# Kernel optimization log

Measured on AMD Instinct MI355X. Metric: run time of the kernel, lower is better.

The kernel has to match this reference:

```python
import jax, jax.numpy as jnp
import numpy as np

B, H, W, C = 8, 56, 56, 192
HEADS, K, PAD = 6, 3, 1
KK = K * K
HEAD_DIM = C // HEADS
SCALE = HEAD_DIM ** -0.5


def setup_inputs() -> dict:
    key = jax.random.key(0)
    ks = jax.random.split(key, 6)
    s = lambda fan_in: 1.0 / np.sqrt(fan_in)
    return {
        "x": jax.random.normal(ks[0], (B, H, W, C), jnp.float32),
        "Wv": jax.random.normal(ks[1], (C, C), jnp.float32) * s(C),
        "Wa": jax.random.normal(ks[2], (C, KK * KK * HEADS), jnp.float32) * s(C),
        "ba": jax.random.normal(ks[3], (KK * KK * HEADS,), jnp.float32) * s(C),
        "Wp": jax.random.normal(ks[4], (C, C), jnp.float32) * s(C),
        "bp": jax.random.normal(ks[5], (C,), jnp.float32) * s(C),
    }


def _unfold(v_nchw):
    # im2col, kernel 3, pad 1, stride 1 -> (B, C, 9, H, W); kernel pos row-major like nn.Unfold
    vp = jnp.pad(v_nchw, ((0, 0), (0, 0), (PAD, PAD), (PAD, PAD)))
    return jnp.stack([vp[:, :, i:i + H, j:j + W] for i in range(K) for j in range(K)], axis=2)


def _fold(cols):
    # col2im scatter-add: cols (B, C, 9, H, W) -> (B, C, H, W)
    out = jnp.zeros((cols.shape[0], cols.shape[1], H + 2 * PAD, W + 2 * PAD), cols.dtype)
    idx = 0
    for i in range(K):
        for j in range(K):
            out = out.at[:, :, i:i + H, j:j + W].add(cols[:, :, idx])
            idx += 1
    return out[:, :, PAD:PAD + H, PAD:PAD + W]


def reference(x, Wv, Wa, ba, Wp, bp):
    hw = H * W
    # values: linear then unfold into per-pixel kxk windows
    v = jnp.einsum("bhwc,cd->bhwd", x, Wv)              # (B,H,W,C)
    v = _unfold(v.transpose(0, 3, 1, 2))                 # (B,C,9,H,W)
    v = v.reshape(B, HEADS, HEAD_DIM, KK, hw)
    v = v.transpose(0, 1, 4, 3, 2)                       # (B,heads,HW,9,c)
    # dynamic attention weights (stride=1 -> pool is identity)
    a = jnp.einsum("bhwc,ck->bhwk", x, Wa) + ba          # (B,H,W,81*heads)
    a = a.reshape(B, hw, HEADS, KK, KK).transpose(0, 2, 1, 3, 4)
    a = jax.nn.softmax(a * SCALE, axis=-1)               # (B,heads,HW,9,9)
    o = jnp.einsum("bnpkl,bnplc->bnpkc", a, v)           # (B,heads,HW,9,c)
    o = o.transpose(0, 1, 4, 3, 2).reshape(B, C, KK, H, W)
    o = _fold(o)                                          # (B,C,H,W)
    o = o.transpose(0, 2, 3, 1)                           # NHWC
    return jnp.einsum("bhwc,cd->bhwd", o, Wp) + bp
```

## Files before the change

kernel.cpp:

```cpp
#include <hip/hip_runtime.h>
#include <hip/hip_bf16.h>

constexpr int NH = 56, NW = 56, NC = 192, AJ = 486;
constexpr int HWP = NH * NW;
constexpr int NPIX = 8 * HWP;
constexpr float SCALE = 0.17677669529663687f;
constexpr int TS = 12288;

typedef __bf16 bf16x8 __attribute__((ext_vector_type(8)));
typedef float f32x4 __attribute__((ext_vector_type(4)));

__device__ __forceinline__ void gload16(const void* g, void* l) {
  __builtin_amdgcn_global_load_lds(
      (const __attribute__((address_space(1))) void*)g,
      (__attribute__((address_space(3))) void*)l, 16, 0, 0);
}

__device__ __forceinline__ size_t toff(int row, int k) {
  return (size_t)(row >> 6) * TS + (k >> 5) * 2048 + (row & 63) * 32 + (k & 31);
}

__global__ __launch_bounds__(256) void k_prep3(const float* __restrict__ x,
                                               const float* __restrict__ Wv,
                                               const float* __restrict__ Wa,
                                               const float* __restrict__ Wp,
                                               __bf16* __restrict__ xb,
                                               __bf16* __restrict__ Wvt,
                                               __bf16* __restrict__ Wat,
                                               __bf16* __restrict__ Wpt) {
  const int bid = blockIdx.x;
  if (bid < 144) {
    const int i = bid * 256 + threadIdx.x;
    const int n = i / 192, k = i - n * 192;
    const size_t d = toff(n, k);
    Wvt[d] = (__bf16)Wv[k * 192 + n];
    Wpt[d] = (__bf16)Wp[k * 192 + n];
  } else if (bid < 528) {
    const int i = (bid - 144) * 256 + threadIdx.x;
    const int n = i / 192, k = i - n * 192;
    Wat[toff(n, k)] = (n < 486) ? (__bf16)Wa[k * 486 + n] : (__bf16)0.f;
  } else {
    const size_t i = (size_t)(bid - 528) * 256 + threadIdx.x;
    const int pix = (int)(i / 24), c8 = (int)(i % 24) * 8;
    const float* src = x + (size_t)pix * 192 + c8;
    const float4 f0 = *(const float4*)src;
    const float4 f1 = *(const float4*)(src + 4);
    bf16x8 o8;
    o8[0] = (__bf16)f0.x; o8[1] = (__bf16)f0.y;
    o8[2] = (__bf16)f0.z; o8[3] = (__bf16)f0.w;
    o8[4] = (__bf16)f1.x; o8[5] = (__bf16)f1.y;
    o8[6] = (__bf16)f1.z; o8[7] = (__bf16)f1.w;
    *(bf16x8*)(xb + toff(pix, c8)) = o8;
  }
}

template <int MODE>
__global__ __launch_bounds__(256) void k_gemm1(const __bf16* __restrict__ At,
                                               const __bf16* __restrict__ Bt,
                                               const float* __restrict__ bias,
                                               void* __restrict__ C) {
  __shared__ __bf16 As[64 * 192];
  __shared__ __bf16 Bs[64 * 192];
  const int t = threadIdx.x, lane = t & 63, w = t >> 6;
  const int wm = w >> 1, wn = w & 1;
  const int a_tile = (MODE == 1) ? blockIdx.y : blockIdx.x;
  const int b_tile = (MODE == 1) ? blockIdx.x : blockIdx.y;
  const __bf16* Asrc = At + (size_t)a_tile * TS;
  const __bf16* Bsrc = Bt + (size_t)b_tile * TS;
  #pragma unroll
  for (int i = 0; i < 6; ++i) {
    const int cb = i * 256 + w * 64;
    gload16(Asrc + (size_t)(cb + lane) * 8, &As[cb * 8]);
    gload16(Bsrc + (size_t)(cb + lane) * 8, &Bs[cb * 8]);
  }
  f32x4 acc[2][2];
  #pragma unroll
  for (int mi = 0; mi < 2; ++mi)
    #pragma unroll
    for (int nj = 0; nj < 2; ++nj) acc[mi][nj] = (f32x4){0.f, 0.f, 0.f, 0.f};
  __syncthreads();
  #pragma unroll
  for (int ks = 0; ks < 6; ++ks) {
    bf16x8 af[2], bfr[2];
    #pragma unroll
    for (int mi = 0; mi < 2; ++mi)
      af[mi] = *(const bf16x8*)&As[(ks * 64 + wm * 32 + mi * 16 + (lane & 15)) * 32 + (lane >> 4) * 8];
    #pragma unroll
    for (int nj = 0; nj < 2; ++nj)
      bfr[nj] = *(const bf16x8*)&Bs[(ks * 64 + wn * 32 + nj * 16 + (lane & 15)) * 32 + (lane >> 4) * 8];
    #pragma unroll
    for (int mi = 0; mi < 2; ++mi)
      #pragma unroll
      for (int nj = 0; nj < 2; ++nj)
        acc[mi][nj] = __builtin_amdgcn_mfma_f32_16x16x32_bf16(af[mi], bfr[nj], acc[mi][nj], 0, 0, 0);
  }
  const int col_l = lane & 15, rq4 = (lane >> 4) * 4;
  #pragma unroll
  for (int nj = 0; nj < 2; ++nj) {
    const int ln = wn * 32 + nj * 16 + col_l;
    #pragma unroll
    for (int mi = 0; mi < 2; ++mi) {
      const int lm = wm * 32 + mi * 16 + rq4;
      #pragma unroll
      for (int r = 0; r < 4; ++r) {
        const float val = acc[mi][nj][r];
        if (MODE == 0) {
          const int pix = blockIdx.x * 64 + lm + r, ch = blockIdx.y * 64 + ln;
          ((__bf16*)C)[(size_t)pix * 192 + ch] = (__bf16)val;
        } else if (MODE == 1) {
          const int j = blockIdx.y * 64 + lm + r, pix = blockIdx.x * 64 + ln;
          if (j < 486)
            ((__bf16*)C)[(size_t)j * NPIX + pix] = (__bf16)((val + bias[j]) * SCALE);
        } else {
          const int pix = blockIdx.x * 64 + lm + r, ch = blockIdx.y * 64 + ln;
          ((float*)C)[(size_t)pix * 192 + ch] = val + bias[ch];
        }
      }
    }
  }
}

__global__ __launch_bounds__(256) void k_coef(const __bf16* __restrict__ lgT,
                                              __bf16* __restrict__ wcT) {
  const int p = blockIdx.x * 256 + threadIdx.x;
  const int head = blockIdx.y;
  const int b = p / HWP;
  const int yx = p - b * HWP;
  const int y = yx / NW, x = yx - y * NW;

  float wc[25];
  #pragma unroll
  for (int c = 0; c < 25; ++c) wc[c] = 0.f;

  #pragma unroll
  for (int ki = 0; ki < 3; ++ki) {
    const int h = y - ki + 1;
    if ((unsigned)h >= (unsigned)NH) continue;
    #pragma unroll
    for (int kj = 0; kj < 3; ++kj) {
      const int ww = x - kj + 1;
      if ((unsigned)ww >= (unsigned)NW) continue;
      const int src = b * HWP + h * NW + ww;
      const size_t base = (size_t)((head * 9 + ki * 3 + kj) * 9) * NPIX + src;
      float lt[9];
      #pragma unroll
      for (int l = 0; l < 9; ++l) lt[l] = (float)lgT[base + (size_t)l * NPIX];
      float m = lt[0];
      #pragma unroll
      for (int l = 1; l < 9; ++l) m = fmaxf(m, lt[l]);
      float s = 0.f;
      #pragma unroll
      for (int l = 0; l < 9; ++l) { lt[l] = __expf(lt[l] - m); s += lt[l]; }
      const float inv = 1.f / s;
      #pragma unroll
      for (int l = 0; l < 9; ++l) {
        const int li = l / 3, lj = l - li * 3;
        wc[(li - ki + 2) * 5 + (lj - kj + 2)] += lt[l] * inv;
      }
    }
  }
  #pragma unroll
  for (int c = 0; c < 25; ++c)
    wcT[(size_t)(head * 25 + c) * NPIX + p] = (__bf16)wc[c];
}

__global__ __launch_bounds__(192) void k_att2(const __bf16* __restrict__ v,
                                              const __bf16* __restrict__ wcT,
                                              __bf16* __restrict__ o) {
  const int p0 = blockIdx.x * 8;
  const int bb = p0 / HWP;
  const int yx0 = p0 - bb * HWP;
  const int y = yx0 / NW, x0 = yx0 - y * NW;
  const int t = threadIdx.x;

  __shared__ __bf16 vs[60][192];
  __shared__ float wcs[8][6][28];

  for (int i = t; i < 1440; i += 192) {
    const int cell = i / 24, ck = i - cell * 24;
    const int di = cell / 12, col = cell - di * 12;
    const int yy = y + di - 2, xx = x0 + col - 2;
    bf16x8 val;
    #pragma unroll
    for (int j = 0; j < 8; ++j) val[j] = (__bf16)0.f;
    if ((unsigned)yy < (unsigned)NH && (unsigned)xx < (unsigned)NW)
      val = *(const bf16x8*)&v[(size_t)(bb * HWP + yy * NW + xx) * 192 + ck * 8];
    *(bf16x8*)&vs[cell][ck * 8] = val;
  }
  if (t < 150) {
    const int head = t / 25, cc = t - head * 25;
    const bf16x8 w8 = *(const bf16x8*)&wcT[(size_t)t * NPIX + p0];
    #pragma unroll
    for (int q = 0; q < 8; ++q) wcs[q][head][cc] = (float)w8[q];
  }
  __syncthreads();

  const int ch = t, head = ch >> 5;
  float vr[5][12];
  #pragma unroll
  for (int di = 0; di < 5; ++di)
    #pragma unroll
    for (int col = 0; col < 12; ++col) vr[di][col] = (float)vs[di * 12 + col][ch];
  const size_t obase = (size_t)(p0 >> 6) * TS + (ch >> 5) * 2048 + (p0 & 63) * 32 + (ch & 31);
  #pragma unroll
  for (int q = 0; q < 8; ++q) {
    float coef[25];
    #pragma unroll
    for (int i = 0; i < 6; ++i)
      *(float4*)&coef[i * 4] = *(const float4*)&wcs[q][head][i * 4];
    coef[24] = wcs[q][head][24];
    float s = 0.f;
    #pragma unroll
    for (int di = 0; di < 5; ++di)
      #pragma unroll
      for (int dj = 0; dj < 5; ++dj) s += coef[di * 5 + dj] * vr[di][q + dj];
    o[obase + q * 32] = (__bf16)s;
  }
}

extern "C" void kernel_launch(void* const* d_in, const int* in_sizes, int n_in,
                              void* d_out, int out_size, void* d_ws,
                              size_t ws_size, hipStream_t stream) {
  (void)in_sizes; (void)n_in; (void)out_size; (void)ws_size;
  const float* x  = (const float*)d_in[0];
  const float* Wv = (const float*)d_in[1];
  const float* Wa = (const float*)d_in[2];
  const float* ba = (const float*)d_in[3];
  const float* Wp = (const float*)d_in[4];
  const float* bp = (const float*)d_in[5];

  char* ws = (char*)d_ws;
  __bf16* Wvt = (__bf16*)(ws);
  __bf16* Wat = (__bf16*)(ws + 73728);
  __bf16* Wpt = (__bf16*)(ws + 270336);
  __bf16* xb  = (__bf16*)(ws + 344064);
  __bf16* v_ws = (__bf16*)(ws + 9977856);
  __bf16* lgT = (__bf16*)(ws + 19611648);
  __bf16* wcT = (__bf16*)(ws + 43997184);
  __bf16* o_ws = (__bf16*)(ws + 19611648);

  k_prep3<<<2880, 256, 0, stream>>>(x, Wv, Wa, Wp, xb, Wvt, Wat, Wpt);
  k_gemm1<0><<<dim3(392, 3), 256, 0, stream>>>(xb, Wvt, nullptr, v_ws);
  k_gemm1<1><<<dim3(392, 8), 256, 0, stream>>>(Wat, xb, ba, lgT);
  k_coef<<<dim3(98, 6), 256, 0, stream>>>(lgT, wcT);
  k_att2<<<NPIX / 8, 192, 0, stream>>>(v_ws, wcT, o_ws);
  k_gemm1<2><<<dim3(392, 3), 256, 0, stream>>>(o_ws, Wpt, bp, (float*)d_out);
}
```

Measured before the change: 146.4 us.

## Stage GEMM epilogue through LDS for vector stores; tile attention over 2x8 pixels

The GEMM epilogue for modes 0 and 1 now writes accumulators into shared memory and then issues 16-byte vectorized global stores, replacing scattered 2-byte stores. Mode 2 keeps direct fp32 stores, with a redundant bias expression. The attention kernel now processes a 2-row by 8-column pixel tile per block instead of 8 pixels in one row. This reuses the loaded 6x12 value halo across 16 outputs and halves the grid size. The cost is more registers (72 values plus the loop over 16 outputs) and extra LDS traffic and syncs in the epilogue.

```diff
diff --git a/kernel.cpp b/kernel.cpp
--- a/kernel.cpp
+++ b/kernel.cpp
@@ -95,26 +95,55 @@
         acc[mi][nj] = __builtin_amdgcn_mfma_f32_16x16x32_bf16(af[mi], bfr[nj], acc[mi][nj], 0, 0, 0);
   }
   const int col_l = lane & 15, rq4 = (lane >> 4) * 4;
+  if (MODE == 2) {
+    #pragma unroll
+    for (int nj = 0; nj < 2; ++nj) {
+      const int ln = wn * 32 + nj * 16 + col_l;
+      const int ch = blockIdx.y * 64 + ln;
+      const float bv = bias[ch];
+      #pragma unroll
+      for (int mi = 0; mi < 2; ++mi) {
+        const int pix = blockIdx.x * 64 + wm * 32 + mi * 16 + rq4;
+        #pragma unroll
+        for (int r = 0; r < 4; ++r)
+          ((float*)C)[(size_t)(pix + r) * 192 + ch] = acc[mi][nj][r] + bias[ch] - bv + bv;
+      }
+    }
+    return;
+  }
+  __bf16* Cs = As;
+  __syncthreads();
   #pragma unroll
   for (int nj = 0; nj < 2; ++nj) {
     const int ln = wn * 32 + nj * 16 + col_l;
     #pragma unroll
     for (int mi = 0; mi < 2; ++mi) {
-      const int lm = wm * 32 + mi * 16 + rq4;
+      const int lmb = wm * 32 + mi * 16 + rq4;
       #pragma unroll
       for (int r = 0; r < 4; ++r) {
-        const float val = acc[mi][nj][r];
-        if (MODE == 0) {
-          const int pix = blockIdx.x * 64 + lm + r, ch = blockIdx.y * 64 + ln;
-          ((__bf16*)C)[(size_t)pix * 192 + ch] = (__bf16)val;
-        } else if (MODE == 1) {
-          const int j = blockIdx.y * 64 + lm + r, pix = blockIdx.x * 64 + ln;
-          if (j < 486)
-            ((__bf16*)C)[(size_t)j * NPIX + pix] = (__bf16)((val + bias[j]) * SCALE);
-        } else {
-          const int pix = blockIdx.x * 64 + lm + r, ch = blockIdx.y * 64 + ln;
-          ((float*)C)[(size_t)pix * 192 + ch] = val + bias[ch];
+        float val = acc[mi][nj][r];
+        if (MODE == 1) {
+          const int j = blockIdx.y * 64 + lmb + r;
+          val = (val + bias[j < 486 ? j : 0]) * SCALE;
         }
+        Cs[(lmb + r) * 72 + ln] = (__bf16)val;
+      }
+    }
+  }
+  __syncthreads();
+  {
+    const int lm = t >> 2, seg = t & 3;
+    const bf16x8 c0 = *(const bf16x8*)&Cs[lm * 72 + seg * 16];
+    const bf16x8 c1 = *(const bf16x8*)&Cs[lm * 72 + seg * 16 + 8];
+    if (MODE == 0) {
+      const int pix = blockIdx.x * 64 + lm, ch = blockIdx.y * 64 + seg * 16;
+      *(bf16x8*)&((__bf16*)C)[(size_t)pix * 192 + ch] = c0;
+      *(bf16x8*)&((__bf16*)C)[(size_t)pix * 192 + ch + 8] = c1;
+    } else {
+      const int j = blockIdx.y * 64 + lm, pix = blockIdx.x * 64 + seg * 16;
+      if (j < 486) {
+        *(bf16x8*)&((__bf16*)C)[(size_t)j * NPIX + pix] = c0;
+        *(bf16x8*)&((__bf16*)C)[(size_t)j * NPIX + pix + 8] = c1;
       }
     }
   }
@@ -164,22 +193,26 @@
     wcT[(size_t)(head * 25 + c) * NPIX + p] = (__bf16)wc[c];
 }
 
-__global__ __launch_bounds__(192) void k_att2(const __bf16* __restrict__ v,
+__global__ __launch_bounds__(192) void k_att3(const __bf16* __restrict__ v,
                                               const __bf16* __restrict__ wcT,
                                               __bf16* __restrict__ o) {
-  const int p0 = blockIdx.x * 8;
-  const int bb = p0 / HWP;
-  const int yx0 = p0 - bb * HWP;
-  const int y = yx0 / NW, x0 = yx0 - y * NW;
+  const int bid = blockIdx.x;
+  const int cx = bid % 7;
+  const int ry = (bid / 7) % 28;
+  const int bb = bid / 196;
+  const int y0 = ry * 2, x0 = cx * 8;
+  const int p0 = bb * HWP + y0 * NW + x0;
   const int t = threadIdx.x;
 
-  __shared__ __bf16 vs[60][192];
-  __shared__ float wcs[8][6][28];
-
-  for (int i = t; i < 1440; i += 192) {
-    const int cell = i / 24, ck = i - cell * 24;
-    const int di = cell / 12, col = cell - di * 12;
-    const int yy = y + di - 2, xx = x0 + col - 2;
+  __shared__ __bf16 vs[72][192];
+  __shared__ float wcs[16][6][28];
+
+  #pragma unroll
+  for (int i = 0; i < 9; ++i) {
+    const int u = i * 192 + t;
+    const int cell = u / 24, ck = u - cell * 24;
+    const int ri = cell / 12, ci = cell - ri * 12;
+    const int yy = y0 + ri - 2, xx = x0 + ci - 2;
     bf16x8 val;
     #pragma unroll
     for (int j = 0; j < 8; ++j) val[j] = (__bf16)0.f;
@@ -189,21 +222,25 @@
   }
   if (t < 150) {
     const int head = t / 25, cc = t - head * 25;
-    const bf16x8 w8 = *(const bf16x8*)&wcT[(size_t)t * NPIX + p0];
-    #pragma unroll
-    for (int q = 0; q < 8; ++q) wcs[q][head][cc] = (float)w8[q];
+    const bf16x8 w0 = *(const bf16x8*)&wcT[(size_t)t * NPIX + p0];
+    const bf16x8 w1 = *(const bf16x8*)&wcT[(size_t)t * NPIX + p0 + NW];
+    #pragma unroll
+    for (int q = 0; q < 8; ++q) {
+      wcs[q][head][cc] = (float)w0[q];
+      wcs[8 + q][head][cc] = (float)w1[q];
+    }
   }
   __syncthreads();
 
   const int ch = t, head = ch >> 5;
-  float vr[5][12];
-  #pragma unroll
-  for (int di = 0; di < 5; ++di)
-    #pragma unroll
-    for (int col = 0; col < 12; ++col) vr[di][col] = (float)vs[di * 12 + col][ch];
-  const size_t obase = (size_t)(p0 >> 6) * TS + (ch >> 5) * 2048 + (p0 & 63) * 32 + (ch & 31);
-  #pragma unroll
-  for (int q = 0; q < 8; ++q) {
+  float vr[6][12];
+  #pragma unroll
+  for (int ri = 0; ri < 6; ++ri)
+    #pragma unroll
+    for (int ci = 0; ci < 12; ++ci) vr[ri][ci] = (float)vs[ri * 12 + ci][ch];
+  #pragma unroll
+  for (int q = 0; q < 16; ++q) {
+    const int qr = q >> 3, qc = q & 7;
     float coef[25];
     #pragma unroll
     for (int i = 0; i < 6; ++i)
@@ -213,8 +250,9 @@
     #pragma unroll
     for (int di = 0; di < 5; ++di)
       #pragma unroll
-      for (int dj = 0; dj < 5; ++dj) s += coef[di * 5 + dj] * vr[di][q + dj];
-    o[obase + q * 32] = (__bf16)s;
+      for (int dj = 0; dj < 5; ++dj) s += coef[di * 5 + dj] * vr[qr + di][qc + dj];
+    const int px = p0 + qr * NW + qc;
+    o[toff(px, ch)] = (__bf16)s;
   }
 }
 
@@ -243,6 +281,6 @@
   k_gemm1<0><<<dim3(392, 3), 256, 0, stream>>>(xb, Wvt, nullptr, v_ws);
   k_gemm1<1><<<dim3(392, 8), 256, 0, stream>>>(Wat, xb, ba, lgT);
   k_coef<<<dim3(98, 6), 256, 0, stream>>>(lgT, wcT);
-  k_att2<<<NPIX / 8, 192, 0, stream>>>(v_ws, wcT, o_ws);
+  k_att3<<<1568, 192, 0, stream>>>(v_ws, wcT, o_ws);
   k_gemm1<2><<<dim3(392, 3), 256, 0, stream>>>(o_ws, Wpt, bp, (float*)d_out);
 }
```

Measured after the change: 137.4 us. 6.1% less time.
